# Kernel tuning notes

Hardware: AMD Instinct MI355X
Metric: run time of the kernel (lower is better)

Reference implementation:

```python
import jax, jax.numpy as jnp
import numpy as np

S, B, L = 64, 32, 64          # seq_len (messages), batch (convs), max tokens per message
V, D = 32000, 300             # vocab, embedding dim
H = 512                       # hidden_dim; per-direction message hidden = H//2
F = 16                        # num_game_features
Hh = H // 2


def lstm_dir(x, mask, Wih, Whh, b, reverse=False):
    """Masked (packed-equivalent) LSTM. x:(T,N,D), mask:(T,N) bool.
    Returns h:(T,N,H) with zeros at invalid steps (matches pad_packed_sequence)."""
    if reverse:
        x, mask = x[::-1], mask[::-1]
    N = x.shape[1]
    Hd = Whh.shape[1]
    xg = jnp.einsum('tnd,gd->tng', x, Wih) + b  # (T,N,4H) input gates precomputed

    def step(carry, inp):
        h, c = carry
        xg_t, m = inp
        g = xg_t + h @ Whh.T
        i, f, gg, o = jnp.split(g, 4, axis=-1)
        c_new = jax.nn.sigmoid(f) * c + jax.nn.sigmoid(i) * jnp.tanh(gg)
        h_new = jax.nn.sigmoid(o) * jnp.tanh(c_new)
        m = m[:, None]
        return (jnp.where(m, h_new, h), jnp.where(m, c_new, c)), jnp.where(m, h_new, 0.0)

    init = (jnp.zeros((N, Hd), x.dtype), jnp.zeros((N, Hd), x.dtype))
    _, hs = jax.lax.scan(step, init, (xg, mask))
    if reverse:
        hs = hs[::-1]
    return hs


def setup_inputs() -> dict:
    key = jax.random.key(0)
    ks = jax.random.split(key, 16)
    s = 1.0 / np.sqrt(Hh)
    sc = 1.0 / np.sqrt(H)
    inp = {
        'messages': jax.random.randint(ks[0], (S, B, L), 0, V),
        'game_features': jax.random.normal(ks[1], (S, B, F), jnp.float32),
        'conv_lengths': jax.random.randint(ks[2], (B,), 1, S + 1),
        'E': jax.random.normal(ks[3], (V, D), jnp.float32) * 0.1,  # frozen embedding
        # message bi-LSTM (forward dir)
        'Wih_f': jax.random.uniform(ks[4], (4 * Hh, D), jnp.float32, -s, s),
        'Whh_f': jax.random.uniform(ks[5], (4 * Hh, Hh), jnp.float32, -s, s),
        'b_f': jax.random.uniform(ks[6], (4 * Hh,), jnp.float32, -s, s),
        # message bi-LSTM (backward dir)
        'Wih_b': jax.random.uniform(ks[7], (4 * Hh, D), jnp.float32, -s, s),
        'Whh_b': jax.random.uniform(ks[8], (4 * Hh, Hh), jnp.float32, -s, s),
        'b_b': jax.random.uniform(ks[9], (4 * Hh,), jnp.float32, -s, s),
        # conversation LSTM
        'Wih_c': jax.random.uniform(ks[10], (4 * H, H), jnp.float32, -sc, sc),
        'Whh_c': jax.random.uniform(ks[11], (4 * H, H), jnp.float32, -sc, sc),
        'b_c': jax.random.uniform(ks[12], (4 * H,), jnp.float32, -sc, sc),
        # classifier
        'Wc': jax.random.uniform(ks[13], (H + F,), jnp.float32, -sc, sc),
        'bc': jax.random.uniform(ks[14], (), jnp.float32, -sc, sc),
    }
    return inp


def reference(messages, game_features, conv_lengths, E, Wih_f, Whh_f, b_f,
              Wih_b, Whh_b, b_b, Wih_c, Whh_c, b_c, Wc, bc):
    # ---- message level: all S*B messages in one batched bi-LSTM pass ----
    flat = messages.reshape(S * B, L)                       # (N, L)
    emb = E[flat]                                           # (N, L, D)
    msg_len = jnp.maximum((flat != 0).sum(1), 1)            # clamp(min=1)
    tmask = jnp.arange(L)[:, None] < msg_len[None, :]       # (L, N)
    x = emb.transpose(1, 0, 2)                              # (L, N, D) time-major
    h_fwd = lstm_dir(x, tmask, Wih_f, Whh_f, b_f, reverse=False)
    h_bwd = lstm_dir(x, tmask, Wih_b, Whh_b, b_b, reverse=True)
    h = jnp.concatenate([h_fwd, h_bwd], axis=-1)            # (L, N, H); zeros at pad
    enc = h.max(axis=0)                                     # maxpool incl. zero pads (torch semantics)
    enc = enc.reshape(S, B, H)
    # ---- conversation level ----
    cmask = jnp.arange(S)[:, None] < conv_lengths[None, :]  # (S, B)
    conv_out = lstm_dir(enc, cmask, Wih_c, Whh_c, b_c)      # (S, B, H), zeros past length
    # dropout is identity at inference
    combined = jnp.concatenate([conv_out, game_features], axis=2)  # (S, B, H+F)
    logits = combined @ Wc + bc                             # (S, B)
    return logits
```

## Files before the change

kernel.cpp:

```cpp
#include <hip/hip_runtime.h>
#include <cmath>

#define S_DIM 64
#define B_DIM 32
#define L_DIM 64
#define NMSG  2048
#define D_DIM 300
#define HH    256
#define HC    512
#define F_DIM 16
#define VOCAB 32000

#define OFF_XGV   0u
#define OFF_WHH   32768000u
#define OFF_WPI   33030144u
#define OFF_WCI   33357824u
#define OFF_WCR   33882112u
#define OFF_ENCB  34406400u
#define OFF_HCONV 34930688u
#define OFF_CCONV 34938880u
#define OFF_CO    34955264u
#define OFF_MLEN  36003840u

typedef __attribute__((ext_vector_type(8))) short s8v;
typedef __attribute__((ext_vector_type(4))) float f4v;
#define MFMA(a,b,c) __builtin_amdgcn_mfma_f32_16x16x32_bf16((a),(b),(c),0,0,0)

__device__ __forceinline__ unsigned short f2bf(float x) {
    unsigned u = __float_as_uint(x);
    return (unsigned short)((u + 0x7FFFu + ((u >> 16) & 1u)) >> 16);
}
__device__ __forceinline__ float bf2f(unsigned short u) {
    return __uint_as_float(((unsigned)u) << 16);
}
__device__ __forceinline__ float sigm(float x) { return 1.0f / (1.0f + __expf(-x)); }
__device__ __forceinline__ float tanh_f(float x) { return 1.0f - 2.0f / (1.0f + __expf(2.0f * x)); }

__device__ __forceinline__ void gload16(const unsigned short* g, unsigned short* l) {
    __builtin_amdgcn_global_load_lds(
        (const __attribute__((address_space(1))) unsigned int*)g,
        (__attribute__((address_space(3))) unsigned int*)l, 16, 0, 0);
}

__global__ __launch_bounds__(256) void pack_whh(
    const float* __restrict__ Whh_f, const float* __restrict__ Whh_b,
    unsigned short* __restrict__ Wp)
{
    int wv = blockIdx.x >> 3, kt = blockIdx.x & 7, dir = blockIdx.y;
    const float* W = dir ? Whh_b : Whh_f;
    int tid = threadIdx.x, lane = tid & 63, iq = tid >> 6;
    int n_l = lane & 15;
    int k0 = kt * 32 + (lane >> 4) * 8;
    #pragma unroll
    for (int ii = 0; ii < 2; ++ii) {
        int i = iq * 2 + ii;
        int nt = (i >> 1) * 16 + wv * 2 + (i & 1);
        int n = nt * 16 + n_l;
        unsigned short tmp[8];
        #pragma unroll
        for (int u = 0; u < 8; ++u) tmp[u] = f2bf(W[(size_t)n * HH + k0 + u]);
        *(uint4*)(Wp + ((size_t)((dir * 8 + wv) * 8 + kt) * 8 + i) * 512 + lane * 8) = *(uint4*)tmp;
    }
}

__global__ __launch_bounds__(256) void pack_wih(
    const float* __restrict__ Wih_f, const float* __restrict__ Wih_b,
    unsigned short* __restrict__ wpi)
{
    int nt = blockIdx.x, dir = blockIdx.y;
    const float* W = dir ? Wih_b : Wih_f;
    int tid = threadIdx.x, lane = tid & 63, ktq = tid >> 6;
    int n = nt * 16 + (lane & 15);
    int kb = (lane >> 4) * 8;
    for (int kt = ktq; kt < 10; kt += 4) {
        int k0 = kt * 32 + kb;
        unsigned short tmp[8];
        #pragma unroll
        for (int u = 0; u < 8; ++u) {
            int k = k0 + u;
            tmp[u] = (k < D_DIM) ? f2bf(W[(size_t)n * D_DIM + k]) : (unsigned short)0;
        }
        *(uint4*)(wpi + (size_t)dir * 327680 + ((size_t)(nt * 10 + kt)) * 512 + lane * 8) = *(uint4*)tmp;
    }
}

__global__ __launch_bounds__(256) void pack_whc(
    const float* __restrict__ Wih_c, const float* __restrict__ Whh_c,
    unsigned short* __restrict__ whci, unsigned short* __restrict__ whcr)
{
    int nt = blockIdx.x, which = blockIdx.y;
    const float* W = which ? Whh_c : Wih_c;
    unsigned short* dst = which ? whcr : whci;
    int tid = threadIdx.x, lane = tid & 63;
    int row = nt * 16 + (lane & 15);
    int kb = (lane >> 4) * 8;
    for (int kt = tid >> 6; kt < 16; kt += 4) {
        int k0 = kt * 32 + kb;
        unsigned short tmp[8];
        #pragma unroll
        for (int u = 0; u < 8; ++u) tmp[u] = f2bf(W[(size_t)row * HC + k0 + u]);
        *(uint4*)(dst + ((size_t)(nt * 16 + kt)) * 512 + lane * 8) = *(uint4*)tmp;
    }
}

__global__ __launch_bounds__(256) void msg_len_kernel(const int* __restrict__ msgs,
                                                      int* __restrict__ mlen) {
    int n = blockIdx.x * 256 + threadIdx.x;
    if (n >= NMSG) return;
    int cnt = 0;
    #pragma unroll 8
    for (int l = 0; l < L_DIM; ++l) cnt += (msgs[n * L_DIM + l] != 0);
    mlen[n] = max(cnt, 1);
}

__global__ __launch_bounds__(256) void init_conv(float* __restrict__ ws) {
    unsigned i = blockIdx.x * 256u + threadIdx.x;
    if (i < 24576u) ws[OFF_HCONV + i] = 0.0f;
}

#define EROW 328
__global__ __launch_bounds__(256) void xg_gemm(
    const float* __restrict__ E,
    const float* __restrict__ b_f, const float* __restrict__ b_b,
    const unsigned short* __restrict__ wpi,
    unsigned short* __restrict__ xgv)
{
    __shared__ __align__(16) unsigned short e_lds[32 * EROW];
    const int w0 = blockIdx.x * 32;
    const int dirb = blockIdx.y >> 2;
    const int jt = blockIdx.y & 3;
    const float* bias = dirb ? b_b : b_f;

    const int tid = threadIdx.x, lane = tid & 63, wv = tid >> 6;
    const int l15 = lane & 15, kg = lane >> 4;

    for (int i = tid; i < 32 * 320; i += 256) {
        int r = i / 320, k = i - r * 320;
        float v = (k < D_DIM) ? E[(size_t)(w0 + r) * D_DIM + k] : 0.0f;
        e_lds[r * EROW + k] = f2bf(v);
    }
    __syncthreads();

    const unsigned short* wb = wpi + (size_t)dirb * 327680;
    const f4v zf = {0.0f, 0.0f, 0.0f, 0.0f};
    f4v acc[2][4];
    #pragma unroll
    for (int m = 0; m < 2; ++m)
        #pragma unroll
        for (int g = 0; g < 4; ++g) acc[m][g] = zf;

    for (int kt = 0; kt < 10; ++kt) {
        s8v a0 = *(const s8v*)&e_lds[l15 * EROW + kt * 32 + kg * 8];
        s8v a1 = *(const s8v*)&e_lds[(16 + l15) * EROW + kt * 32 + kg * 8];
        #pragma unroll
        for (int g = 0; g < 4; ++g) {
            int nt = g * 16 + jt * 4 + wv;
            s8v b = *(const s8v*)(wb + ((size_t)(nt * 10 + kt)) * 512 + lane * 8);
            acc[0][g] = MFMA(a0, b, acc[0][g]);
            acc[1][g] = MFMA(a1, b, acc[1][g]);
        }
    }

    const int j = jt * 64 + wv * 16 + l15;
    float bv[4];
    #pragma unroll
    for (int g = 0; g < 4; ++g) bv[g] = bias[g * 256 + j];
    const int colp = (jt * 2 + (wv >> 1)) * 128 + l15 * 8 + (wv & 1) * 4;
    #pragma unroll
    for (int m = 0; m < 2; ++m)
        #pragma unroll
        for (int r = 0; r < 4; ++r) {
            int w = w0 + m * 16 + kg * 4 + r;
            unsigned short t4[4];
            #pragma unroll
            for (int g = 0; g < 4; ++g) t4[g] = f2bf(acc[m][g][r] + bv[g]);
            *(uint2*)(xgv + ((size_t)dirb * VOCAB + w) * 1024 + colp) = *(uint2*)t4;
        }
}

#define XGS  1032
#define HROW 264
__global__ __launch_bounds__(512, 2) void word_lstm(
    const int* __restrict__ msgs, const int* __restrict__ mlen,
    const unsigned short* __restrict__ xgv,
    const unsigned short* __restrict__ whh,
    unsigned short* __restrict__ enc_bf)
{
    __shared__ __align__(16) unsigned short xg_lds[2][16 * XGS];
    __shared__ __align__(16) unsigned short h_lds[2][16 * HROW];
    __shared__ int tok_s[16 * 64];
    __shared__ int len_s[16];

    const int mg = blockIdx.x >> 1, dir = blockIdx.x & 1;
    const int tid = threadIdx.x, lane = tid & 63, wv = tid >> 6;
    const int l15 = lane & 15, kg = lane >> 4;

    for (int i = tid; i < 16 * 64; i += 512) tok_s[i] = msgs[mg * 1024 + i];
    if (tid < 16) len_s[tid] = mlen[mg * 16 + tid];
    for (int i = tid; i < 2 * 16 * HROW; i += 512) h_lds[0][i] = 0;
    __syncthreads();

    const unsigned short* xv = xgv + (size_t)dir * VOCAB * 1024;

    const unsigned short* wbase = whh + (size_t)(dir * 8 + wv) * 32768 + lane * 8;
    const unsigned short* bp[16];
    #pragma unroll
    for (int jj = 0; jj < 16; ++jj) bp[jj] = wbase + jj * 2048;

    int lens[4];
    #pragma unroll
    for (int r = 0; r < 4; ++r) lens[r] = len_s[kg * 4 + r];

    int bmax = 1;
    #pragma unroll
    for (int i = 0; i < 16; ++i) bmax = max(bmax, len_s[i]);

    float c_st[2][4], rm[2][4];
    unsigned short hbf[2][4];
    #pragma unroll
    for (int q = 0; q < 2; ++q)
        #pragma unroll
        for (int r = 0; r < 4; ++r) { c_st[q][r] = 0.0f; rm[q][r] = -INFINITY; hbf[q][r] = 0; }

    #pragma unroll
    for (int rr = 0; rr < 2; ++rr) {
        int row = wv * 2 + rr;
        int tt = dir ? (len_s[row] - 1) : 0;
        if (tt < 0) tt = 0;
        const unsigned short* src = xv + (size_t)tok_s[row * 64 + tt] * 1024 + lane * 8;
        gload16(src,       &xg_lds[0][row * XGS]);
        gload16(src + 512, &xg_lds[0][row * XGS + 512]);
    }

    for (int t = 0; t < bmax; ++t) {
        __syncthreads();
        const int buf = t & 1;
        const int hbuf = t & 1;

        if (t + 1 < bmax) {
            #pragma unroll
            for (int rr = 0; rr < 2; ++rr) {
                int row = wv * 2 + rr;
                int tn = t + 1;
                int tt = dir ? (len_s[row] - 1 - tn) : tn;
                if (tt < 0) tt = 0;
                const unsigned short* src = xv + (size_t)tok_s[row * 64 + tt] * 1024 + lane * 8;
                gload16(src,       &xg_lds[buf ^ 1][row * XGS]);
                gload16(src + 512, &xg_lds[buf ^ 1][row * XGS + 512]);
            }
        }

        f4v acc[2][4];
        {
            s8v v8[4];
            #pragma unroll
            for (int r = 0; r < 4; ++r)
                v8[r] = *(const s8v*)&xg_lds[buf][(kg * 4 + r) * XGS + wv * 128 + l15 * 8];
            #pragma unroll
            for (int q = 0; q < 2; ++q)
                #pragma unroll
                for (int g = 0; g < 4; ++g) {
                    f4v v;
                    #pragma unroll
                    for (int r = 0; r < 4; ++r)
                        v[r] = bf2f((unsigned short)v8[r][q * 4 + g]);
                    acc[q][g] = v;
                }
        }

        #pragma unroll
        for (int kt = 0; kt < 8; ++kt) {
            s8v a = *(const s8v*)&h_lds[hbuf][l15 * HROW + kt * 32 + kg * 8];
            const unsigned short* pA = bp[kt * 2];
            const unsigned short* pB = bp[kt * 2 + 1];
            acc[0][0] = MFMA(a, *(const s8v*)(pA),        acc[0][0]);
            acc[1][0] = MFMA(a, *(const s8v*)(pA + 512),  acc[1][0]);
            acc[0][1] = MFMA(a, *(const s8v*)(pA + 1024), acc[0][1]);
            acc[1][1] = MFMA(a, *(const s8v*)(pA + 1536), acc[1][1]);
            acc[0][2] = MFMA(a, *(const s8v*)(pB),        acc[0][2]);
            acc[1][2] = MFMA(a, *(const s8v*)(pB + 512),  acc[1][2]);
            acc[0][3] = MFMA(a, *(const s8v*)(pB + 1024), acc[0][3]);
            acc[1][3] = MFMA(a, *(const s8v*)(pB + 1536), acc[1][3]);
        }

        #pragma unroll
        for (int q = 0; q < 2; ++q)
            #pragma unroll
            for (int r = 0; r < 4; ++r) {
                float gi = acc[q][0][r], gf = acc[q][1][r], gc = acc[q][2][r], go = acc[q][3][r];
                float cn = sigm(gf) * c_st[q][r] + sigm(gi) * tanh_f(gc);
                float hn = sigm(go) * tanh_f(cn);
                if (t < lens[r]) {
                    c_st[q][r] = cn;
                    rm[q][r] = fmaxf(rm[q][r], hn);
                    hbf[q][r] = f2bf(hn);
                }
                h_lds[hbuf ^ 1][(kg * 4 + r) * HROW + wv * 32 + q * 16 + l15] = hbf[q][r];
            }
    }

    #pragma unroll
    for (int q = 0; q < 2; ++q)
        #pragma unroll
        for (int r = 0; r < 4; ++r) {
            float v = rm[q][r];
            if (lens[r] < 64) v = fmaxf(v, 0.0f);
            enc_bf[(size_t)(mg * 16 + kg * 4 + r) * HC + dir * HH + wv * 32 + q * 16 + l15] = f2bf(v);
        }
}

#define CROW 520
__global__ __launch_bounds__(256) void xgc_gemm(
    const unsigned short* __restrict__ enc_bf,
    const unsigned short* __restrict__ whci,
    const float* __restrict__ b_c,
    unsigned short* __restrict__ xgc)
{
    __shared__ __align__(16) unsigned short e_lds[32 * CROW];
    const int m0 = blockIdx.x * 32;
    const int n0 = blockIdx.y * 256;
    const int tid = threadIdx.x, lane = tid & 63, wv = tid >> 6;
    const int l15 = lane & 15, kg = lane >> 4;

    for (int i = tid; i < 2048; i += 256) {
        int row = i >> 6, u4 = i & 63;
        ((uint4*)&e_lds[row * CROW])[u4] = ((const uint4*)(enc_bf + (size_t)(m0 + row) * HC))[u4];
    }
    __syncthreads();

    const f4v zf = {0.0f, 0.0f, 0.0f, 0.0f};
    f4v acc[2][4];
    #pragma unroll
    for (int m = 0; m < 2; ++m)
        #pragma unroll
        for (int q = 0; q < 4; ++q) acc[m][q] = zf;

    for (int kt = 0; kt < 16; ++kt) {
        s8v a0 = *(const s8v*)&e_lds[l15 * CROW + kt * 32 + kg * 8];
        s8v a1 = *(const s8v*)&e_lds[(16 + l15) * CROW + kt * 32 + kg * 8];
        #pragma unroll
        for (int q = 0; q < 4; ++q) {
            int nt = (n0 >> 4) + wv * 4 + q;
            s8v b = *(const s8v*)(whci + ((size_t)(nt * 16 + kt)) * 512 + lane * 8);
            acc[0][q] = MFMA(a0, b, acc[0][q]);
            acc[1][q] = MFMA(a1, b, acc[1][q]);
        }
    }

    #pragma unroll
    for (int q = 0; q < 4; ++q) {
        int col = n0 + (wv * 4 + q) * 16 + l15;
        float bv = b_c[col];
        #pragma unroll
        for (int m = 0; m < 2; ++m)
            #pragma unroll
            for (int r = 0; r < 4; ++r)
                xgc[(size_t)(m0 + m * 16 + kg * 4 + r) * 2048 + col] = f2bf(acc[m][q][r] + bv);
    }
}

__global__ __launch_bounds__(256) void conv_step(
    const unsigned short* __restrict__ whcr,
    const unsigned short* __restrict__ xgc,
    const int* __restrict__ conv_len,
    unsigned short* __restrict__ h_bf,
    float* __restrict__ c_ws,
    float* __restrict__ co,
    int s)
{
    __shared__ __align__(16) unsigned short xh[32 * CROW];
    __shared__ float gbuf[4][32][16];

    const int tid = threadIdx.x, jb = blockIdx.x;
    const int lane = tid & 63, g = tid >> 6;
    const int l15 = lane & 15, kg = lane >> 4;

    for (int i = tid; i < 2048; i += 256) {
        int row = i >> 6, u4 = i & 63;
        ((uint4*)&xh[row * CROW])[u4] = ((const uint4*)(h_bf + (size_t)row * HC))[u4];
    }
    __syncthreads();

    const int col = g * 512 + jb * 16 + l15;
    f4v acc0, acc1;
    #pragma unroll
    for (int r = 0; r < 4; ++r) {
        acc0[r] = bf2f(xgc[(size_t)(s * B_DIM + kg * 4 + r) * 2048 + col]);
        acc1[r] = bf2f(xgc[(size_t)(s * B_DIM + 16 + kg * 4 + r) * 2048 + col]);
    }

    const int nt = g * 32 + jb;
    for (int kt = 0; kt < 16; ++kt) {
        s8v a0 = *(const s8v*)&xh[l15 * CROW + kt * 32 + kg * 8];
        s8v a1 = *(const s8v*)&xh[(16 + l15) * CROW + kt * 32 + kg * 8];
        s8v b  = *(const s8v*)(whcr + ((size_t)(nt * 16 + kt)) * 512 + lane * 8);
        acc0 = MFMA(a0, b, acc0);
        acc1 = MFMA(a1, b, acc1);
    }

    #pragma unroll
    for (int r = 0; r < 4; ++r) {
        gbuf[g][kg * 4 + r][l15]      = acc0[r];
        gbuf[g][16 + kg * 4 + r][l15] = acc1[r];
    }
    __syncthreads();

    #pragma unroll
    for (int u = 0; u < 2; ++u) {
        int cell = tid + 256 * u;
        int b = cell >> 4, jj = cell & 15;
        int j = jb * 16 + jj;
        bool valid = s < conv_len[b];
        float g_i = gbuf[0][b][jj], g_f = gbuf[1][b][jj];
        float g_c = gbuf[2][b][jj], g_o = gbuf[3][b][jj];
        float cold = c_ws[b * HC + j];
        float cn = sigm(g_f) * cold + sigm(g_i) * tanh_f(g_c);
        float hn = sigm(g_o) * tanh_f(cn);
        float outv = 0.0f;
        if (valid) {
            c_ws[b * HC + j] = cn;
            h_bf[b * HC + j] = f2bf(hn);
            outv = hn;
        }
        co[((size_t)s * B_DIM + b) * HC + j] = outv;
    }
}

__global__ __launch_bounds__(256) void logits_kernel(
    const float* __restrict__ gfeat, const float* __restrict__ Wc, const float* __restrict__ bc,
    const float* __restrict__ co, float* __restrict__ out)
{
    int o = blockIdx.x * 4 + (threadIdx.x >> 6);
    int lane = threadIdx.x & 63;
    const float* row = co + (size_t)o * HC;
    float sum = 0.0f;
    #pragma unroll
    for (int u = 0; u < 8; ++u) sum += row[lane + 64 * u] * Wc[lane + 64 * u];
    if (lane < F_DIM) sum += gfeat[o * F_DIM + lane] * Wc[HC + lane];
    #pragma unroll
    for (int off = 32; off > 0; off >>= 1) sum += __shfl_down(sum, off, 64);
    if (lane == 0) out[o] = sum + bc[0];
}

extern "C" void kernel_launch(void* const* d_in, const int* in_sizes, int n_in,
                              void* d_out, int out_size, void* d_ws, size_t ws_size,
                              hipStream_t stream) {
    const int*   msgs    = (const int*)  d_in[0];
    const float* gfeat   = (const float*)d_in[1];
    const int*   convlen = (const int*)  d_in[2];
    const float* E       = (const float*)d_in[3];
    const float* Wih_f   = (const float*)d_in[4];
    const float* Whh_f   = (const float*)d_in[5];
    const float* b_f     = (const float*)d_in[6];
    const float* Wih_b   = (const float*)d_in[7];
    const float* Whh_b   = (const float*)d_in[8];
    const float* b_b     = (const float*)d_in[9];
    const float* Wih_c   = (const float*)d_in[10];
    const float* Whh_c   = (const float*)d_in[11];
    const float* b_c     = (const float*)d_in[12];
    const float* Wc      = (const float*)d_in[13];
    const float* bc      = (const float*)d_in[14];
    float* out = (float*)d_out;
    float* ws  = (float*)d_ws;

    unsigned short* xgv    = (unsigned short*)(ws + OFF_XGV);
    unsigned short* xgc    = (unsigned short*)(ws + OFF_XGV);
    unsigned short* whh    = (unsigned short*)(ws + OFF_WHH);
    unsigned short* wpi    = (unsigned short*)(ws + OFF_WPI);
    unsigned short* whci   = (unsigned short*)(ws + OFF_WCI);
    unsigned short* whcr   = (unsigned short*)(ws + OFF_WCR);
    unsigned short* enc_bf = (unsigned short*)(ws + OFF_ENCB);
    unsigned short* h_bf   = (unsigned short*)(ws + OFF_HCONV);
    float*          c_ws   = ws + OFF_CCONV;
    float*          co     = ws + OFF_CO;
    int*            mlen   = (int*)(ws + OFF_MLEN);

    pack_whh<<<dim3(64, 2), 256, 0, stream>>>(Whh_f, Whh_b, whh);
    pack_wih<<<dim3(64, 2), 256, 0, stream>>>(Wih_f, Wih_b, wpi);
    pack_whc<<<dim3(128, 2), 256, 0, stream>>>(Wih_c, Whh_c, whci, whcr);
    msg_len_kernel<<<NMSG / 256, 256, 0, stream>>>(msgs, mlen);
    init_conv<<<96, 256, 0, stream>>>(ws);
    xg_gemm<<<dim3(1000, 8), 256, 0, stream>>>(E, b_f, b_b, wpi, xgv);

    word_lstm<<<256, 512, 0, stream>>>(msgs, mlen, xgv, whh, enc_bf);

    xgc_gemm<<<dim3(64, 8), 256, 0, stream>>>(enc_bf, whci, b_c, xgc);

    for (int s = 0; s < S_DIM; ++s)
        conv_step<<<32, 256, 0, stream>>>(whcr, xgc, convlen, h_bf, c_ws, co, s);

    logits_kernel<<<NMSG / 4, 256, 0, stream>>>(gfeat, Wc, bc, co, out);
}
```

Measured before the change: 1.215 ms.

## Split word LSTM across 16 waves and prefetch gate inputs into registers

The word-level LSTM block grows from 8 to 16 waves, so each wave now owns 16 hidden columns instead of 32. The Whh packing is reorganised to match the new per-wave layout. The LDS staging of the gathered input gates is replaced with direct per-lane register prefetches, double-buffered across a two-step unrolled loop. The aim is to shorten the serial per-step critical path and drop the large LDS buffer, at the cost of more barrier participants and a higher per-block thread count.

```diff
diff --git a/kernel.cpp b/kernel.cpp
--- a/kernel.cpp
+++ b/kernel.cpp
@@ -36,31 +36,20 @@
 __device__ __forceinline__ float sigm(float x) { return 1.0f / (1.0f + __expf(-x)); }
 __device__ __forceinline__ float tanh_f(float x) { return 1.0f - 2.0f / (1.0f + __expf(2.0f * x)); }
 
-__device__ __forceinline__ void gload16(const unsigned short* g, unsigned short* l) {
-    __builtin_amdgcn_global_load_lds(
-        (const __attribute__((address_space(1))) unsigned int*)g,
-        (__attribute__((address_space(3))) unsigned int*)l, 16, 0, 0);
-}
-
 __global__ __launch_bounds__(256) void pack_whh(
     const float* __restrict__ Whh_f, const float* __restrict__ Whh_b,
     unsigned short* __restrict__ Wp)
 {
-    int wv = blockIdx.x >> 3, kt = blockIdx.x & 7, dir = blockIdx.y;
+    int cg = blockIdx.x & 15, kt = blockIdx.x >> 4;
+    int dir = blockIdx.y;
     const float* W = dir ? Whh_b : Whh_f;
-    int tid = threadIdx.x, lane = tid & 63, iq = tid >> 6;
-    int n_l = lane & 15;
+    int tid = threadIdx.x, lane = tid & 63, g = tid >> 6;
+    int wrow = g * 256 + cg * 16 + (lane & 15);
     int k0 = kt * 32 + (lane >> 4) * 8;
-    #pragma unroll
-    for (int ii = 0; ii < 2; ++ii) {
-        int i = iq * 2 + ii;
-        int nt = (i >> 1) * 16 + wv * 2 + (i & 1);
-        int n = nt * 16 + n_l;
-        unsigned short tmp[8];
-        #pragma unroll
-        for (int u = 0; u < 8; ++u) tmp[u] = f2bf(W[(size_t)n * HH + k0 + u]);
-        *(uint4*)(Wp + ((size_t)((dir * 8 + wv) * 8 + kt) * 8 + i) * 512 + lane * 8) = *(uint4*)tmp;
-    }
+    unsigned short tmp[8];
+    #pragma unroll
+    for (int u = 0; u < 8; ++u) tmp[u] = f2bf(W[(size_t)wrow * HH + k0 + u]);
+    *(uint4*)(Wp + ((((size_t)(dir * 16 + cg) * 8 + kt) * 4 + g) * 512) + lane * 8) = *(uint4*)tmp;
 }
 
 __global__ __launch_bounds__(256) void pack_wih(
@@ -178,34 +167,29 @@
         }
 }
 
-#define XGS  1032
 #define HROW 264
-__global__ __launch_bounds__(512, 2) void word_lstm(
+__global__ __launch_bounds__(1024, 4) void word_lstm(
     const int* __restrict__ msgs, const int* __restrict__ mlen,
     const unsigned short* __restrict__ xgv,
     const unsigned short* __restrict__ whh,
     unsigned short* __restrict__ enc_bf)
 {
-    __shared__ __align__(16) unsigned short xg_lds[2][16 * XGS];
     __shared__ __align__(16) unsigned short h_lds[2][16 * HROW];
     __shared__ int tok_s[16 * 64];
     __shared__ int len_s[16];
 
     const int mg = blockIdx.x >> 1, dir = blockIdx.x & 1;
-    const int tid = threadIdx.x, lane = tid & 63, wv = tid >> 6;
+    const int tid = threadIdx.x, lane = tid & 63, cg = tid >> 6;
     const int l15 = lane & 15, kg = lane >> 4;
 
-    for (int i = tid; i < 16 * 64; i += 512) tok_s[i] = msgs[mg * 1024 + i];
+    for (int i = tid; i < 16 * 64; i += 1024) tok_s[i] = msgs[mg * 1024 + i];
     if (tid < 16) len_s[tid] = mlen[mg * 16 + tid];
-    for (int i = tid; i < 2 * 16 * HROW; i += 512) h_lds[0][i] = 0;
+    for (int i = tid; i < 2 * 16 * HROW; i += 1024) ((unsigned short*)h_lds)[i] = 0;
     __syncthreads();
 
     const unsigned short* xv = xgv + (size_t)dir * VOCAB * 1024;
-
-    const unsigned short* wbase = whh + (size_t)(dir * 8 + wv) * 32768 + lane * 8;
-    const unsigned short* bp[16];
-    #pragma unroll
-    for (int jj = 0; jj < 16; ++jj) bp[jj] = wbase + jj * 2048;
+    const unsigned short* wb = whh + (size_t)(dir * 16 + cg) * 16384 + lane * 8;
+    const int qoff = (cg >> 1) * 128 + l15 * 8 + (cg & 1) * 4;
 
     int lens[4];
     #pragma unroll
@@ -215,98 +199,74 @@
     #pragma unroll
     for (int i = 0; i < 16; ++i) bmax = max(bmax, len_s[i]);
 
-    float c_st[2][4], rm[2][4];
-    unsigned short hbf[2][4];
-    #pragma unroll
-    for (int q = 0; q < 2; ++q)
-        #pragma unroll
-        for (int r = 0; r < 4; ++r) { c_st[q][r] = 0.0f; rm[q][r] = -INFINITY; hbf[q][r] = 0; }
-
-    #pragma unroll
-    for (int rr = 0; rr < 2; ++rr) {
-        int row = wv * 2 + rr;
-        int tt = dir ? (len_s[row] - 1) : 0;
-        if (tt < 0) tt = 0;
-        const unsigned short* src = xv + (size_t)tok_s[row * 64 + tt] * 1024 + lane * 8;
-        gload16(src,       &xg_lds[0][row * XGS]);
-        gload16(src + 512, &xg_lds[0][row * XGS + 512]);
-    }
-
-    for (int t = 0; t < bmax; ++t) {
+    float c_st[4], rm[4];
+    unsigned short hbf[4];
+    #pragma unroll
+    for (int r = 0; r < 4; ++r) { c_st[r] = 0.0f; rm[r] = -INFINITY; hbf[r] = 0; }
+
+    auto gather = [&](int t, uint2* q) {
+        #pragma unroll
+        for (int r = 0; r < 4; ++r) {
+            int tt = dir ? (lens[r] - 1 - t) : t;
+            if (tt < 0) tt = 0;
+            q[r] = *(const uint2*)(xv + (size_t)tok_s[(kg * 4 + r) * 64 + tt] * 1024 + qoff);
+        }
+    };
+
+    auto step = [&](int t, uint2* qc, uint2* qn) {
         __syncthreads();
-        const int buf = t & 1;
         const int hbuf = t & 1;
 
-        if (t + 1 < bmax) {
-            #pragma unroll
-            for (int rr = 0; rr < 2; ++rr) {
-                int row = wv * 2 + rr;
-                int tn = t + 1;
-                int tt = dir ? (len_s[row] - 1 - tn) : tn;
-                if (tt < 0) tt = 0;
-                const unsigned short* src = xv + (size_t)tok_s[row * 64 + tt] * 1024 + lane * 8;
-                gload16(src,       &xg_lds[buf ^ 1][row * XGS]);
-                gload16(src + 512, &xg_lds[buf ^ 1][row * XGS + 512]);
-            }
-        }
-
-        f4v acc[2][4];
-        {
-            s8v v8[4];
+        f4v acc[4];
+        #pragma unroll
+        for (int g = 0; g < 4; ++g) {
+            f4v v;
             #pragma unroll
             for (int r = 0; r < 4; ++r)
-                v8[r] = *(const s8v*)&xg_lds[buf][(kg * 4 + r) * XGS + wv * 128 + l15 * 8];
-            #pragma unroll
-            for (int q = 0; q < 2; ++q)
-                #pragma unroll
-                for (int g = 0; g < 4; ++g) {
-                    f4v v;
-                    #pragma unroll
-                    for (int r = 0; r < 4; ++r)
-                        v[r] = bf2f((unsigned short)v8[r][q * 4 + g]);
-                    acc[q][g] = v;
-                }
-        }
+                v[r] = bf2f(((const unsigned short*)&qc[r])[g]);
+            acc[g] = v;
+        }
+
+        if (t + 1 < bmax) gather(t + 1, qn);
 
         #pragma unroll
         for (int kt = 0; kt < 8; ++kt) {
             s8v a = *(const s8v*)&h_lds[hbuf][l15 * HROW + kt * 32 + kg * 8];
-            const unsigned short* pA = bp[kt * 2];
-            const unsigned short* pB = bp[kt * 2 + 1];
-            acc[0][0] = MFMA(a, *(const s8v*)(pA),        acc[0][0]);
-            acc[1][0] = MFMA(a, *(const s8v*)(pA + 512),  acc[1][0]);
-            acc[0][1] = MFMA(a, *(const s8v*)(pA + 1024), acc[0][1]);
-            acc[1][1] = MFMA(a, *(const s8v*)(pA + 1536), acc[1][1]);
-            acc[0][2] = MFMA(a, *(const s8v*)(pB),        acc[0][2]);
-            acc[1][2] = MFMA(a, *(const s8v*)(pB + 512),  acc[1][2]);
-            acc[0][3] = MFMA(a, *(const s8v*)(pB + 1024), acc[0][3]);
-            acc[1][3] = MFMA(a, *(const s8v*)(pB + 1536), acc[1][3]);
-        }
-
-        #pragma unroll
-        for (int q = 0; q < 2; ++q)
-            #pragma unroll
-            for (int r = 0; r < 4; ++r) {
-                float gi = acc[q][0][r], gf = acc[q][1][r], gc = acc[q][2][r], go = acc[q][3][r];
-                float cn = sigm(gf) * c_st[q][r] + sigm(gi) * tanh_f(gc);
-                float hn = sigm(go) * tanh_f(cn);
-                if (t < lens[r]) {
-                    c_st[q][r] = cn;
-                    rm[q][r] = fmaxf(rm[q][r], hn);
-                    hbf[q][r] = f2bf(hn);
-                }
-                h_lds[hbuf ^ 1][(kg * 4 + r) * HROW + wv * 32 + q * 16 + l15] = hbf[q][r];
+            const unsigned short* pw = wb + kt * 2048;
+            acc[0] = MFMA(a, *(const s8v*)(pw),        acc[0]);
+            acc[1] = MFMA(a, *(const s8v*)(pw + 512),  acc[1]);
+            acc[2] = MFMA(a, *(const s8v*)(pw + 1024), acc[2]);
+            acc[3] = MFMA(a, *(const s8v*)(pw + 1536), acc[3]);
+        }
+
+        #pragma unroll
+        for (int r = 0; r < 4; ++r) {
+            float gi = acc[0][r], gf = acc[1][r], gc = acc[2][r], go = acc[3][r];
+            float cn = sigm(gf) * c_st[r] + sigm(gi) * tanh_f(gc);
+            float hn = sigm(go) * tanh_f(cn);
+            if (t < lens[r]) {
+                c_st[r] = cn;
+                rm[r] = fmaxf(rm[r], hn);
+                hbf[r] = f2bf(hn);
             }
-    }
-
-    #pragma unroll
-    for (int q = 0; q < 2; ++q)
-        #pragma unroll
-        for (int r = 0; r < 4; ++r) {
-            float v = rm[q][r];
-            if (lens[r] < 64) v = fmaxf(v, 0.0f);
-            enc_bf[(size_t)(mg * 16 + kg * 4 + r) * HC + dir * HH + wv * 32 + q * 16 + l15] = f2bf(v);
-        }
+            h_lds[hbuf ^ 1][(kg * 4 + r) * HROW + cg * 16 + l15] = hbf[r];
+        }
+    };
+
+    uint2 qA[4], qB[4];
+    gather(0, qA);
+    for (int t = 0; t < bmax; t += 2) {
+        step(t, qA, qB);
+        if (t + 1 >= bmax) break;
+        step(t + 1, qB, qA);
+    }
+
+    #pragma unroll
+    for (int r = 0; r < 4; ++r) {
+        float v = rm[r];
+        if (lens[r] < 64) v = fmaxf(v, 0.0f);
+        enc_bf[(size_t)(mg * 16 + kg * 4 + r) * HC + dir * HH + cg * 16 + l15] = f2bf(v);
+    }
 }
 
 #define CROW 520
@@ -475,14 +435,14 @@
     float*          co     = ws + OFF_CO;
     int*            mlen   = (int*)(ws + OFF_MLEN);
 
-    pack_whh<<<dim3(64, 2), 256, 0, stream>>>(Whh_f, Whh_b, whh);
+    pack_whh<<<dim3(128, 2), 256, 0, stream>>>(Whh_f, Whh_b, whh);
     pack_wih<<<dim3(64, 2), 256, 0, stream>>>(Wih_f, Wih_b, wpi);
     pack_whc<<<dim3(128, 2), 256, 0, stream>>>(Wih_c, Whh_c, whci, whcr);
     msg_len_kernel<<<NMSG / 256, 256, 0, stream>>>(msgs, mlen);
     init_conv<<<96, 256, 0, stream>>>(ws);
     xg_gemm<<<dim3(1000, 8), 256, 0, stream>>>(E, b_f, b_b, wpi, xgv);
 
-    word_lstm<<<256, 512, 0, stream>>>(msgs, mlen, xgv, whh, enc_bf);
+    word_lstm<<<256, 1024, 0, stream>>>(msgs, mlen, xgv, whh, enc_bf);
 
     xgc_gemm<<<dim3(64, 8), 256, 0, stream>>>(enc_bf, whci, b_c, xgc);
 
```

New measurement: 1.267 ms. 4.3% more time.

## Prefetch input gates directly into registers and remap blocks by direction

Applied to the files above, without the earlier changes.

The word-level LSTM no longer stages per-token input-gate rows through a double-buffered LDS tile via global_load_lds. Each lane now issues nontemporal 16-byte loads straight into registers one step ahead and unpacks the bf16 values in place. This removes the LDS traffic and the large shared buffer, which may raise occupancy. Block indices are also remapped so that groups of four blocks share a direction, which may improve cache locality for the recurrent weights. The cost is more live registers holding the prefetched vectors, and the nontemporal hint may reduce cache reuse of the gate table.

```diff
diff --git a/kernel.cpp b/kernel.cpp
--- a/kernel.cpp
+++ b/kernel.cpp
@@ -24,6 +24,7 @@
 
 typedef __attribute__((ext_vector_type(8))) short s8v;
 typedef __attribute__((ext_vector_type(4))) float f4v;
+typedef __attribute__((ext_vector_type(4))) unsigned int u4v;
 #define MFMA(a,b,c) __builtin_amdgcn_mfma_f32_16x16x32_bf16((a),(b),(c),0,0,0)
 
 __device__ __forceinline__ unsigned short f2bf(float x) {
@@ -35,12 +36,6 @@
 }
 __device__ __forceinline__ float sigm(float x) { return 1.0f / (1.0f + __expf(-x)); }
 __device__ __forceinline__ float tanh_f(float x) { return 1.0f - 2.0f / (1.0f + __expf(2.0f * x)); }
-
-__device__ __forceinline__ void gload16(const unsigned short* g, unsigned short* l) {
-    __builtin_amdgcn_global_load_lds(
-        (const __attribute__((address_space(1))) unsigned int*)g,
-        (__attribute__((address_space(3))) unsigned int*)l, 16, 0, 0);
-}
 
 __global__ __launch_bounds__(256) void pack_whh(
     const float* __restrict__ Whh_f, const float* __restrict__ Whh_b,
@@ -178,7 +173,6 @@
         }
 }
 
-#define XGS  1032
 #define HROW 264
 __global__ __launch_bounds__(512, 2) void word_lstm(
     const int* __restrict__ msgs, const int* __restrict__ mlen,
@@ -186,30 +180,33 @@
     const unsigned short* __restrict__ whh,
     unsigned short* __restrict__ enc_bf)
 {
-    __shared__ __align__(16) unsigned short xg_lds[2][16 * XGS];
     __shared__ __align__(16) unsigned short h_lds[2][16 * HROW];
     __shared__ int tok_s[16 * 64];
     __shared__ int len_s[16];
 
-    const int mg = blockIdx.x >> 1, dir = blockIdx.x & 1;
-    const int tid = threadIdx.x, lane = tid & 63, wv = tid >> 6;
+    const int bid = blockIdx.x;
+    const int dir = (bid >> 2) & 1;
+    const int mg  = (bid & 3) | ((bid >> 3) << 2);
+    const int tid = threadIdx.x, lane = tid & 63, cg = tid >> 6;
     const int l15 = lane & 15, kg = lane >> 4;
 
     for (int i = tid; i < 16 * 64; i += 512) tok_s[i] = msgs[mg * 1024 + i];
     if (tid < 16) len_s[tid] = mlen[mg * 16 + tid];
-    for (int i = tid; i < 2 * 16 * HROW; i += 512) h_lds[0][i] = 0;
+    for (int i = tid; i < 2 * 16 * HROW; i += 512) ((unsigned short*)h_lds)[i] = 0;
     __syncthreads();
 
     const unsigned short* xv = xgv + (size_t)dir * VOCAB * 1024;
 
-    const unsigned short* wbase = whh + (size_t)(dir * 8 + wv) * 32768 + lane * 8;
+    const unsigned short* wbase = whh + (size_t)(dir * 8 + cg) * 32768 + lane * 8;
     const unsigned short* bp[16];
     #pragma unroll
     for (int jj = 0; jj < 16; ++jj) bp[jj] = wbase + jj * 2048;
 
-    int lens[4];
-    #pragma unroll
-    for (int r = 0; r < 4; ++r) lens[r] = len_s[kg * 4 + r];
+    const int qoff = cg * 128 + l15 * 8;
+
+    int lens[4], rb[4];
+    #pragma unroll
+    for (int r = 0; r < 4; ++r) { lens[r] = len_s[kg * 4 + r]; rb[r] = (kg * 4 + r) * 64; }
 
     int bmax = 1;
     #pragma unroll
@@ -222,51 +219,43 @@
         #pragma unroll
         for (int r = 0; r < 4; ++r) { c_st[q][r] = 0.0f; rm[q][r] = -INFINITY; hbf[q][r] = 0; }
 
-    #pragma unroll
-    for (int rr = 0; rr < 2; ++rr) {
-        int row = wv * 2 + rr;
-        int tt = dir ? (len_s[row] - 1) : 0;
+    u4v qc[4], qn[4];
+    #pragma unroll
+    for (int r = 0; r < 4; ++r) {
+        int tt = dir ? (lens[r] - 1) : 0;
         if (tt < 0) tt = 0;
-        const unsigned short* src = xv + (size_t)tok_s[row * 64 + tt] * 1024 + lane * 8;
-        gload16(src,       &xg_lds[0][row * XGS]);
-        gload16(src + 512, &xg_lds[0][row * XGS + 512]);
+        qc[r] = __builtin_nontemporal_load((const u4v*)(xv + (size_t)tok_s[rb[r] + tt] * 1024 + qoff));
+        qn[r] = qc[r];
     }
 
     for (int t = 0; t < bmax; ++t) {
         __syncthreads();
-        const int buf = t & 1;
         const int hbuf = t & 1;
 
         if (t + 1 < bmax) {
             #pragma unroll
-            for (int rr = 0; rr < 2; ++rr) {
-                int row = wv * 2 + rr;
-                int tn = t + 1;
-                int tt = dir ? (len_s[row] - 1 - tn) : tn;
+            for (int r = 0; r < 4; ++r) {
+                int tt = dir ? (lens[r] - 2 - t) : (t + 1);
                 if (tt < 0) tt = 0;
-                const unsigned short* src = xv + (size_t)tok_s[row * 64 + tt] * 1024 + lane * 8;
-                gload16(src,       &xg_lds[buf ^ 1][row * XGS]);
-                gload16(src + 512, &xg_lds[buf ^ 1][row * XGS + 512]);
+                qn[r] = __builtin_nontemporal_load((const u4v*)(xv + (size_t)tok_s[rb[r] + tt] * 1024 + qoff));
             }
         }
 
         f4v acc[2][4];
-        {
-            s8v v8[4];
+        #pragma unroll
+        for (int q = 0; q < 2; ++q)
             #pragma unroll
-            for (int r = 0; r < 4; ++r)
-                v8[r] = *(const s8v*)&xg_lds[buf][(kg * 4 + r) * XGS + wv * 128 + l15 * 8];
-            #pragma unroll
-            for (int q = 0; q < 2; ++q)
+            for (int g = 0; g < 4; ++g) {
+                const int e = q * 4 + g;
+                f4v v;
                 #pragma unroll
-                for (int g = 0; g < 4; ++g) {
-                    f4v v;
-                    #pragma unroll
-                    for (int r = 0; r < 4; ++r)
-                        v[r] = bf2f((unsigned short)v8[r][q * 4 + g]);
-                    acc[q][g] = v;
+                for (int r = 0; r < 4; ++r) {
+                    unsigned w = qc[r][e >> 1];
+                    v[r] = (e & 1) ? __uint_as_float(w & 0xFFFF0000u)
+                                   : __uint_as_float(w << 16);
                 }
-        }
+                acc[q][g] = v;
+            }
 
         #pragma unroll
         for (int kt = 0; kt < 8; ++kt) {
@@ -295,8 +284,11 @@
                     rm[q][r] = fmaxf(rm[q][r], hn);
                     hbf[q][r] = f2bf(hn);
                 }
-                h_lds[hbuf ^ 1][(kg * 4 + r) * HROW + wv * 32 + q * 16 + l15] = hbf[q][r];
+                h_lds[hbuf ^ 1][(kg * 4 + r) * HROW + cg * 32 + q * 16 + l15] = hbf[q][r];
             }
+
+        #pragma unroll
+        for (int r = 0; r < 4; ++r) qc[r] = qn[r];
     }
 
     #pragma unroll
@@ -305,7 +297,7 @@
         for (int r = 0; r < 4; ++r) {
             float v = rm[q][r];
             if (lens[r] < 64) v = fmaxf(v, 0.0f);
-            enc_bf[(size_t)(mg * 16 + kg * 4 + r) * HC + dir * HH + wv * 32 + q * 16 + l15] = f2bf(v);
+            enc_bf[(size_t)(mg * 16 + kg * 4 + r) * HC + dir * HH + cg * 32 + q * 16 + l15] = f2bf(v);
         }
 }
 
```

Measured after the change: 1.423 ms. 1.17x slower.
